# Optimization experiments

Hardware: AMD Instinct MI355X
Metric: run time of the kernel (lower is better)

## Reference

```python
import jax, jax.numpy as jnp
import numpy as np

N_NODES = 51200
N_GRAPHS = 64
NODES_PER_GRAPH = 800
N_EDGES = 819200
DIM_IN = 128
DIM_HIDDEN = 64
HEADS = 3
DIM_OUT = 64


def leaky(x, slope):
    return jnp.where(x >= 0, x, slope * x)


def setup_inputs() -> dict:
    key = jax.random.key(0)
    ks = jax.random.split(key, 12)
    s = lambda fan_in: 1.0 / np.sqrt(fan_in)
    X = jax.random.normal(ks[0], (N_NODES, DIM_IN), dtype=jnp.float32)
    edge_indices = jax.random.randint(ks[1], (2, N_EDGES), 0, N_NODES, dtype=jnp.int32)
    ptr = (jnp.arange(N_GRAPHS + 1, dtype=jnp.int32) * NODES_PER_GRAPH)
    # linearSeq: Linear(dim_in, dim_hidden) + LeakyReLU
    W1 = jax.random.uniform(ks[2], (DIM_IN, DIM_HIDDEN), jnp.float32, -s(DIM_IN), s(DIM_IN))
    b1 = jax.random.uniform(ks[3], (DIM_HIDDEN,), jnp.float32, -s(DIM_IN), s(DIM_IN))
    # GATConv params: lin_src/lin_dst (no bias), att_src/att_dst, bias (concat=False -> out_channels)
    W_src = jax.random.uniform(ks[4], (DIM_HIDDEN, HEADS * DIM_HIDDEN), jnp.float32, -s(DIM_HIDDEN), s(DIM_HIDDEN))
    W_dst = jax.random.uniform(ks[5], (DIM_HIDDEN, HEADS * DIM_HIDDEN), jnp.float32, -s(DIM_HIDDEN), s(DIM_HIDDEN))
    att_src = jax.random.normal(ks[6], (HEADS, DIM_HIDDEN), dtype=jnp.float32) * 0.1
    att_dst = jax.random.normal(ks[7], (HEADS, DIM_HIDDEN), dtype=jnp.float32) * 0.1
    gat_bias = jnp.zeros((DIM_HIDDEN,), dtype=jnp.float32)
    # linear_final: Linear(2*dim_hidden, dim_out)
    Wf = jax.random.uniform(ks[8], (2 * DIM_HIDDEN, DIM_OUT), jnp.float32, -s(2 * DIM_HIDDEN), s(2 * DIM_HIDDEN))
    bf = jax.random.uniform(ks[9], (DIM_OUT,), jnp.float32, -s(2 * DIM_HIDDEN), s(2 * DIM_HIDDEN))
    return {"X": X, "W1": W1, "b1": b1, "W_src": W_src, "W_dst": W_dst,
            "att_src": att_src, "att_dst": att_dst, "gat_bias": gat_bias,
            "Wf": Wf, "bf": bf, "edge_indices": edge_indices, "ptr": ptr}


def reference(X, W1, b1, W_src, W_dst, att_src, att_dst, gat_bias, Wf, bf, edge_indices, ptr):
    N = X.shape[0]
    src, dst = edge_indices[0], edge_indices[1]  # message flows src -> dst
    # input projection
    h = leaky(X @ W1 + b1, 0.01)                                  # [N, DH]
    # GATConv (heads=3, concat=False, add_self_loops=False)
    x_src = (h @ W_src).reshape(N, HEADS, DIM_HIDDEN)             # [N, H, C]
    x_dst = (h @ W_dst).reshape(N, HEADS, DIM_HIDDEN)
    a_src = jnp.einsum('nhc,hc->nh', x_src, att_src)              # [N, H]
    a_dst = jnp.einsum('nhc,hc->nh', x_dst, att_dst)
    logits = leaky(a_src[src] + a_dst[dst], 0.2)                  # [E, H]
    # segment softmax over incoming edges of each target node
    m = jax.ops.segment_max(logits, dst, num_segments=N)          # [N, H]
    e = jnp.exp(logits - m[dst])
    denom = jax.ops.segment_sum(e, dst, num_segments=N)           # [N, H]
    attn = e / denom[dst]                                         # [E, H]
    msg = x_src[src] * attn[..., None]                            # [E, H, C]
    agg = jax.ops.segment_sum(msg, dst, num_segments=N)           # [N, H, C]
    out = agg.mean(axis=1) + gat_bias                             # concat=False -> head mean
    # final head
    cat = jnp.concatenate([h, out], axis=1)                       # [N, 2*DH]
    y = leaky(cat, 0.01) @ Wf + bf                                # [N, DO]
    # aggregate_using_ptr: mean-pool nodes per graph using CSR ptr
    node_graph = jnp.searchsorted(ptr, jnp.arange(N), side='right') - 1
    sums = jax.ops.segment_sum(y, node_graph, num_segments=ptr.shape[0] - 1)
    counts = (ptr[1:] - ptr[:-1]).astype(y.dtype)
    pooled = sums / counts[:, None]                               # [n_graphs, DO]
    return pooled, attn
```

## Files before the change

### kernel.cpp

```cpp
#include <hip/hip_runtime.h>
#include <hip/hip_bf16.h>

#define N_NODES   51200
#define N_GRAPHS  64
#define N_EDGES   819200
#define DIM_IN    128
#define DH        64
#define HEADS     3
#define DIM_OUT   64
#define CAP       96
#define NPART     8
#define PART_SZ   (N_NODES / NPART)
#define PBUF_CAP  131072
#define BIN_BLOCKS  (N_EDGES / 2048)
#define PREP_BLOCKS 116
#define SC2_BLOCKS  (NPART * (PBUF_CAP / 2048))
#define K1_BLOCKS   (N_NODES / 64)

typedef __hip_bfloat16 bf16;
typedef short bf16x8 __attribute__((ext_vector_type(8)));
typedef float f32x4  __attribute__((ext_vector_type(4)));

__device__ __forceinline__ float b2f(bf16 x) { return __bfloat162float(x); }
__device__ __forceinline__ bf16  f2b(float x) { return __float2bfloat16(x); }
__device__ __forceinline__ short f2bs(float x) { return (short)__bfloat16_as_ushort(f2b(x)); }
__device__ __forceinline__ float leaky(float x, float s) { return x >= 0.f ? x : s * x; }
__device__ __forceinline__ float ldin(const void* p, size_t i, int f32) {
    return f32 ? ((const float*)p)[i] : b2f(((const bf16*)p)[i]);
}
__device__ __forceinline__ bf16x8 ld8(const void* p, size_t i, int f32) {
    if (!f32) return *((const bf16x8*)((const short*)p + i));
    const float* f = (const float*)p + i;
    bf16x8 r;
    #pragma unroll
    for (int j = 0; j < 8; ++j) r[j] = f2bs(f[j]);
    return r;
}

__global__ __launch_bounds__(256) void detect_kernel(const unsigned short* __restrict__ Xu,
                                                     int* __restrict__ flag) {
    __shared__ int cnt;
    int tid = threadIdx.x;
    if (tid == 0) cnt = 0;
    __syncthreads();
    int local = 0;
    for (int i = tid * 2; i < 8192; i += 512) {
        unsigned e = (Xu[i] >> 7) & 0xFF;
        if (e >= 110 && e <= 135) local++;
    }
    atomicAdd(&cnt, local);
    __syncthreads();
    if (tid == 0) *flag = (cnt < 2048) ? 1 : 0;
}

__global__ __launch_bounds__(256) void k_bin_prep(const int* __restrict__ src,
                                                  const int* __restrict__ dst,
                                                  int* __restrict__ pcur,
                                                  unsigned* __restrict__ pbuf,
                                                  const void* __restrict__ W1,
                                                  const void* __restrict__ Wsrc,
                                                  const void* __restrict__ Wdst,
                                                  const void* __restrict__ Wf,
                                                  const void* __restrict__ att_src,
                                                  const void* __restrict__ att_dst,
                                                  const int* __restrict__ flagp,
                                                  short* __restrict__ W1t,
                                                  short* __restrict__ Wspt,
                                                  short* __restrict__ Wft,
                                                  short* __restrict__ Wat) {
    if (blockIdx.x < BIN_BLOCKS) {
        __shared__ int cnt[NPART];
        __shared__ int base[NPART];
        const int tid = threadIdx.x;
        if (tid < NPART) cnt[tid] = 0;
        __syncthreads();
        const int e0 = blockIdx.x * 2048;
        unsigned pk[8]; int pp[8]; int rr[8];
        #pragma unroll
        for (int t = 0; t < 8; ++t) {
            int e = e0 + t * 256 + tid;
            int s = src[e], d = dst[e];
            int p = d / PART_SZ;
            pk[t] = ((unsigned)s << 16) | (unsigned)d;
            pp[t] = p;
            rr[t] = atomicAdd(&cnt[p], 1);
        }
        __syncthreads();
        if (tid < NPART) base[tid] = atomicAdd(&pcur[tid], cnt[tid]);
        __syncthreads();
        #pragma unroll
        for (int t = 0; t < 8; ++t) {
            int p = pp[t];
            int o = base[p] + rr[t];
            if (o < PBUF_CAP) pbuf[(size_t)p * PBUF_CAP + o] = pk[t];
        }
        return;
    }
    const int f32 = *flagp;
    int idx = (blockIdx.x - BIN_BLOCKS) * 256 + threadIdx.x;
    if (idx < 8192) {
        int n = idx >> 7, k = idx & 127;
        W1t[idx] = f2bs(ldin(W1, (size_t)k * 64 + n, f32));
    } else if (idx < 20480) {
        int j = idx - 8192;
        int col = j / 192;
        int rem = j - col * 192;
        int hh = rem >> 6, kk = rem & 63;
        Wspt[j] = f2bs(ldin(Wsrc, (size_t)kk * 192 + hh * 64 + col, f32) * (1.0f / 3.0f));
    } else if (idx < 28672) {
        int j = idx - 20480;
        int n = j >> 7, k = j & 127;
        Wft[j] = f2bs(ldin(Wf, (size_t)k * 64 + n, f32));
    } else if (idx < 29696) {
        int j = idx - 28672;
        int n = j >> 6, k = j & 63;
        float v = 0.f;
        if (n < 3) {
            for (int c = 0; c < 64; ++c)
                v += ldin(Wsrc, (size_t)k * 192 + n * 64 + c, f32) * ldin(att_src, n * 64 + c, f32);
        } else if (n < 6) {
            for (int c = 0; c < 64; ++c)
                v += ldin(Wdst, (size_t)k * 192 + (n - 3) * 64 + c, f32) * ldin(att_dst, (n - 3) * 64 + c, f32);
        }
        Wat[j] = f2bs(v);
    }
}

__global__ __launch_bounds__(256) void k_scatter_k1(const unsigned* __restrict__ pbuf,
                                                    const int* __restrict__ pcur,
                                                    int* __restrict__ cursor,
                                                    unsigned short* __restrict__ bucket,
                                                    const void* __restrict__ X,
                                                    const short* __restrict__ W1t,
                                                    const short* __restrict__ Wat,
                                                    const void* __restrict__ b1,
                                                    const int* __restrict__ flagp,
                                                    bf16* __restrict__ h_bf,
                                                    unsigned char* __restrict__ h8,
                                                    float* __restrict__ a_src4,
                                                    float* __restrict__ a_dst4) {
    if (blockIdx.x < SC2_BLOCKS) {
        const int p = blockIdx.x & (NPART - 1);
        const int slice = blockIdx.x >> 3;
        const int pc = min(pcur[p], PBUF_CAP);
        const unsigned* pb = pbuf + (size_t)p * PBUF_CAP;
        const int base = slice * 2048 + threadIdx.x;
        #pragma unroll
        for (int t = 0; t < 8; ++t) {
            int i = base + t * 256;
            if (i < pc) {
                unsigned pk = pb[i];
                int d = (int)(pk & 0xFFFFu);
                int pos = atomicAdd(&cursor[d], 1);
                if (pos < CAP) bucket[(size_t)d * CAP + pos] = (unsigned short)(pk >> 16);
            }
        }
        return;
    }
    const int f32 = *flagp;
    __shared__ short hs[64 * 72];
    const int tid  = threadIdx.x;
    const int w    = tid >> 6;
    const int lane = tid & 63;
    const int lm   = lane & 15;
    const int q    = lane >> 4;
    const int row0 = (blockIdx.x - SC2_BLOCKS) * 64;

    const float bias = ldin(b1, w * 16 + lm, f32);
    for (int mt = 0; mt < 4; ++mt) {
        f32x4 acc = {0.f, 0.f, 0.f, 0.f};
        #pragma unroll
        for (int kc = 0; kc < 4; ++kc) {
            bf16x8 a = ld8(X, (size_t)(row0 + mt * 16 + lm) * 128 + kc * 32 + q * 8, f32);
            bf16x8 b = *((const bf16x8*)(W1t + (size_t)(w * 16 + lm) * 128 + kc * 32 + q * 8));
            acc = __builtin_amdgcn_mfma_f32_16x16x32_bf16(a, b, acc, 0, 0, 0);
        }
        #pragma unroll
        for (int r = 0; r < 4; ++r) {
            int row = mt * 16 + q * 4 + r;
            float v = leaky(acc[r] + bias, 0.01f);
            short hv = f2bs(v);
            hs[row * 72 + w * 16 + lm] = hv;
            h_bf[(size_t)(row0 + row) * 64 + w * 16 + lm] = __ushort_as_bfloat16((unsigned short)hv);
            h8[(size_t)(row0 + row) * 64 + w * 16 + lm] =
                (unsigned char)__builtin_amdgcn_cvt_pk_fp8_f32(v, 0.f, 0, false);
        }
    }
    __syncthreads();

    {
        const int mt = w;
        bf16x8 a0  = *((const bf16x8*)(hs + (mt * 16 + lm) * 72 + q * 8));
        bf16x8 a1  = *((const bf16x8*)(hs + (mt * 16 + lm) * 72 + 32 + q * 8));
        bf16x8 b0  = *((const bf16x8*)(Wat + (size_t)lm * 64 + q * 8));
        bf16x8 b1v = *((const bf16x8*)(Wat + (size_t)lm * 64 + 32 + q * 8));
        f32x4 acca = {0.f, 0.f, 0.f, 0.f};
        acca = __builtin_amdgcn_mfma_f32_16x16x32_bf16(a0, b0, acca, 0, 0, 0);
        acca = __builtin_amdgcn_mfma_f32_16x16x32_bf16(a1, b1v, acca, 0, 0, 0);
        if (lm < 6) {
            #pragma unroll
            for (int r = 0; r < 4; ++r) {
                int row = row0 + mt * 16 + q * 4 + r;
                if (lm < 3) a_src4[(size_t)row * 4 + lm] = acca[r];
                else        a_dst4[(size_t)row * 4 + (lm - 3)] = acca[r];
            }
        }
    }
}

__global__ __launch_bounds__(256) void edge_kernel(const unsigned short* __restrict__ bucket,
                                                   const int* __restrict__ cursor,
                                                   const float* __restrict__ a_src4,
                                                   const float* __restrict__ a_dst4,
                                                   const unsigned char* __restrict__ h8,
                                                   float4* __restrict__ dstinfo,
                                                   bf16* __restrict__ wagg) {
    const int lane = threadIdx.x & 63;
    const int w = threadIdx.x >> 6;
    const int n = blockIdx.x * 4 + w;
    const int dg = min(cursor[n], CAP);
    const float4 ad = ((const float4*)a_dst4)[n];
    __shared__ float4 buf[4][64];
    float den0 = 0.f, den1 = 0.f, den2 = 0.f;
    float acc0 = 0.f, acc1 = 0.f, acc2 = 0.f;
    for (int c0 = 0; c0 < dg; c0 += 64) {
        int cnt = min(64, dg - c0);
        if (lane < cnt) {
            int s = bucket[n * CAP + c0 + lane];
            const float4 as = ((const float4*)a_src4)[s];
            float e0 = __expf(leaky(as.x + ad.x, 0.2f));
            float e1 = __expf(leaky(as.y + ad.y, 0.2f));
            float e2 = __expf(leaky(as.z + ad.z, 0.2f));
            den0 += e0; den1 += e1; den2 += e2;
            buf[w][lane] = make_float4(e0, e1, e2, __int_as_float(s));
        }
        asm volatile("s_waitcnt lgkmcnt(0)" ::: "memory");
        int j = 0;
        for (; j + 8 <= cnt; j += 8) {
            float4 r[8]; int hv[8];
            #pragma unroll
            for (int u = 0; u < 8; ++u) r[u] = buf[w][j + u];
            #pragma unroll
            for (int u = 0; u < 8; ++u)
                hv[u] = (int)h8[(((unsigned)__float_as_int(r[u].w)) << 6) | (unsigned)lane];
            #pragma unroll
            for (int u = 0; u < 8; ++u) {
                float f = __builtin_amdgcn_cvt_f32_fp8(hv[u], 0);
                acc0 += r[u].x * f; acc1 += r[u].y * f; acc2 += r[u].z * f;
            }
        }
        for (; j < cnt; ++j) {
            float4 r = buf[w][j];
            int hvv = (int)h8[(((unsigned)__float_as_int(r.w)) << 6) | (unsigned)lane];
            float f = __builtin_amdgcn_cvt_f32_fp8(hvv, 0);
            acc0 += r.x * f; acc1 += r.y * f; acc2 += r.z * f;
        }
    }
    #pragma unroll
    for (int off = 32; off >= 1; off >>= 1) {
        den0 += __shfl_xor(den0, off);
        den1 += __shfl_xor(den1, off);
        den2 += __shfl_xor(den2, off);
    }
    float inv0 = den0 > 0.f ? 1.f / den0 : 0.f;
    float inv1 = den1 > 0.f ? 1.f / den1 : 0.f;
    float inv2 = den2 > 0.f ? 1.f / den2 : 0.f;
    size_t wb = (size_t)n * 192;
    wagg[wb + lane]       = f2b(acc0 * inv0);
    wagg[wb + 64 + lane]  = f2b(acc1 * inv1);
    wagg[wb + 128 + lane] = f2b(acc2 * inv2);
    if (lane == 0) {
        dstinfo[(size_t)n * 2 + 0] = make_float4(ad.x, ad.y, ad.z, 0.f);
        dstinfo[(size_t)n * 2 + 1] = make_float4(inv0, inv1, inv2, 0.f);
    }
}

__global__ __launch_bounds__(256) void attn_g3_kernel(const int* __restrict__ src,
                                                      const int* __restrict__ dst,
                                                      const float* __restrict__ a_src4,
                                                      const float4* __restrict__ dstinfo,
                                                      const bf16* __restrict__ h_bf,
                                                      const bf16* __restrict__ wagg,
                                                      const short* __restrict__ Wspt,
                                                      const short* __restrict__ Wft,
                                                      const void* __restrict__ gat_bias,
                                                      const void* __restrict__ bfv,
                                                      const int* __restrict__ flagp,
                                                      bf16* __restrict__ y_bf,
                                                      void* __restrict__ d_out) {
    const int f32 = *flagp;
    __shared__ short cs[64 * 136];
    if (blockIdx.x < N_EDGES / 256) {
        int e = blockIdx.x * 256 + threadIdx.x;
        int s = src[e], d = dst[e];
        const float4 as = ((const float4*)a_src4)[s];
        const float4 ad = dstinfo[(size_t)d * 2 + 0];
        const float4 cv = dstinfo[(size_t)d * 2 + 1];
        float a0 = __expf(leaky(as.x + ad.x, 0.2f)) * cv.x;
        float a1 = __expf(leaky(as.y + ad.y, 0.2f)) * cv.y;
        float a2 = __expf(leaky(as.z + ad.z, 0.2f)) * cv.z;
        size_t o = (size_t)N_GRAPHS * DIM_OUT + (size_t)e * 3;
        if (f32) {
            float* p = (float*)d_out;
            p[o] = a0; p[o + 1] = a1; p[o + 2] = a2;
        } else {
            bf16* p = (bf16*)d_out;
            p[o] = f2b(a0); p[o + 1] = f2b(a1); p[o + 2] = f2b(a2);
        }
        return;
    }
    const int bid  = blockIdx.x - N_EDGES / 256;
    const int tid  = threadIdx.x;
    const int w    = tid >> 6;
    const int lane = tid & 63;
    const int lm   = lane & 15;
    const int q    = lane >> 4;
    const int row0 = bid * 64;
    for (int idx = tid; idx < 64 * 64; idx += 256) {
        int r = idx >> 6, k = idx & 63;
        cs[r * 136 + k] = f2bs(leaky(b2f(h_bf[(size_t)(row0 + r) * 64 + k]), 0.01f));
    }
    {
        const int col = w * 16 + lm;
        const float gb = ldin(gat_bias, col, f32);
        for (int mt = 0; mt < 4; ++mt) {
            f32x4 acc = {0.f, 0.f, 0.f, 0.f};
            #pragma unroll
            for (int kc = 0; kc < 6; ++kc) {
                bf16x8 a = *((const bf16x8*)((const short*)wagg + (size_t)(row0 + mt * 16 + lm) * 192 + kc * 32 + q * 8));
                bf16x8 b = *((const bf16x8*)(Wspt + (size_t)col * 192 + kc * 32 + q * 8));
                acc = __builtin_amdgcn_mfma_f32_16x16x32_bf16(a, b, acc, 0, 0, 0);
            }
            #pragma unroll
            for (int r = 0; r < 4; ++r) {
                int row = mt * 16 + q * 4 + r;
                cs[row * 136 + 64 + col] = f2bs(leaky(acc[r] + gb, 0.01f));
            }
        }
    }
    __syncthreads();
    const float bias = ldin(bfv, w * 16 + lm, f32);
    for (int mt = 0; mt < 4; ++mt) {
        f32x4 acc = {0.f, 0.f, 0.f, 0.f};
        #pragma unroll
        for (int kc = 0; kc < 4; ++kc) {
            bf16x8 a = *((const bf16x8*)(cs + (mt * 16 + lm) * 136 + kc * 32 + q * 8));
            bf16x8 b = *((const bf16x8*)(Wft + (size_t)(w * 16 + lm) * 128 + kc * 32 + q * 8));
            acc = __builtin_amdgcn_mfma_f32_16x16x32_bf16(a, b, acc, 0, 0, 0);
        }
        #pragma unroll
        for (int r = 0; r < 4; ++r) {
            int row = row0 + mt * 16 + q * 4 + r;
            y_bf[(size_t)row * 64 + w * 16 + lm] = f2b(acc[r] + bias);
        }
    }
}

__global__ __launch_bounds__(1024) void pool_kernel(const bf16* __restrict__ y_bf,
                                                    const int* __restrict__ ptr,
                                                    const int* __restrict__ flagp,
                                                    void* __restrict__ d_out) {
    __shared__ float part[16][64];
    const int f32 = *flagp;
    const int g = blockIdx.x;
    const int w = threadIdx.x >> 6, lane = threadIdx.x & 63;
    const int lo = ptr[g], hi = ptr[g + 1];
    const int cnt = hi - lo;
    float s = 0.f;
    for (int i = lo + w; i < hi; i += 16) s += b2f(y_bf[(size_t)i * DIM_OUT + lane]);
    part[w][lane] = s;
    __syncthreads();
    if (threadIdx.x < 64) {
        float t = 0.f;
        #pragma unroll
        for (int k = 0; k < 16; ++k) t += part[k][threadIdx.x];
        float v = t / (float)cnt;
        if (f32) ((float*)d_out)[g * DIM_OUT + threadIdx.x] = v;
        else     ((bf16*)d_out)[g * DIM_OUT + threadIdx.x]  = f2b(v);
    }
}

extern "C" void kernel_launch(void* const* d_in, const int* in_sizes, int n_in,
                              void* d_out, int out_size, void* d_ws, size_t ws_size,
                              hipStream_t stream) {
    const void* X        = d_in[0];
    const void* W1       = d_in[1];
    const void* b1       = d_in[2];
    const void* Wsrc     = d_in[3];
    const void* Wdst     = d_in[4];
    const void* att_src  = d_in[5];
    const void* att_dst  = d_in[6];
    const void* gat_bias = d_in[7];
    const void* Wf       = d_in[8];
    const void* bfv      = d_in[9];
    const int*  ei       = (const int*)d_in[10];
    const int*  ptr      = (const int*)d_in[11];
    const int*  src  = ei;
    const int*  dstp = ei + N_EDGES;

    char* ws = (char*)d_ws;
    size_t off_b = 0;
    auto alloc = [&](size_t bytes) -> char* {
        char* p = ws + off_b;
        off_b += (bytes + 255) & ~(size_t)255;
        return p;
    };
    int*     flag    = (int*)    alloc(256);
    short*   W1t     = (short*)  alloc(8192 * 2);
    short*   Wspt    = (short*)  alloc(12288 * 2);
    short*   Wft     = (short*)  alloc(8192 * 2);
    short*   Wat     = (short*)  alloc(1024 * 2);
    bf16*    h_bf    = (bf16*)   alloc((size_t)N_NODES * 64 * 2);
    unsigned char* h8 = (unsigned char*)alloc((size_t)N_NODES * 64);
    float*   a_src4  = (float*)  alloc((size_t)N_NODES * 16);
    float*   a_dst4  = (float*)  alloc((size_t)N_NODES * 16);
    float4*  dstinfo = (float4*) alloc((size_t)N_NODES * 2 * 16);
    bf16*    wagg    = (bf16*)   alloc((size_t)N_NODES * 192 * 2);
    int*     pcur    = (int*)    alloc(256);
    int*     cursor  = (int*)    alloc((size_t)N_NODES * 4);
    unsigned short* bucket = (unsigned short*)alloc((size_t)N_NODES * CAP * 2);
    unsigned* pbuf   = (unsigned*)wagg;
    bf16*    y_bf    = (bf16*)   bucket;
    if (off_b > ws_size) return;

    hipLaunchKernelGGL(detect_kernel, dim3(1), dim3(256), 0, stream,
                       (const unsigned short*)X, flag);
    hipMemsetAsync(pcur, 0, 256 + (size_t)N_NODES * 4, stream);
    hipLaunchKernelGGL(k_bin_prep, dim3(BIN_BLOCKS + PREP_BLOCKS), dim3(256), 0, stream,
                       src, dstp, pcur, pbuf,
                       W1, Wsrc, Wdst, Wf, att_src, att_dst, flag, W1t, Wspt, Wft, Wat);
    hipLaunchKernelGGL(k_scatter_k1, dim3(SC2_BLOCKS + K1_BLOCKS), dim3(256), 0, stream,
                       pbuf, pcur, cursor, bucket,
                       X, W1t, Wat, b1, flag, h_bf, h8, a_src4, a_dst4);
    hipLaunchKernelGGL(edge_kernel, dim3(N_NODES / 4), dim3(256), 0, stream,
                       bucket, cursor, a_src4, a_dst4, h8, dstinfo, wagg);
    hipLaunchKernelGGL(attn_g3_kernel, dim3(N_EDGES / 256 + N_NODES / 64), dim3(256), 0, stream,
                       src, dstp, a_src4, dstinfo, h_bf, wagg, Wspt, Wft,
                       gat_bias, bfv, flag, y_bf, d_out);
    hipLaunchKernelGGL(pool_kernel, dim3(N_GRAPHS), dim3(1024), 0, stream, y_bf, ptr, flag, d_out);
}
```

Baseline: 237.1 us.

## Fuse pooling into final GEMM, merge detect kernel, use LDS counters for scatter

The input-dtype detection moves into the prep blocks of the binning kernel, using a per-block __syncthreads_count plus one extra block that writes the global flag, so the separate detect launch goes away. Edge binning now uses 64 partitions, and each scatter block bins its partition with LDS atomic counters before writing the cursor array, replacing global atomics and the cursor memset. Mean pooling is fused into the final linear stage through per-graph atomic partial sums and a done-counter, so the last block for each graph writes the output. This removes the y_bf round trip and the pool kernel, but adds float atomics, order-dependent summation, and a scatter phase with only 64 blocks.

```diff
diff --git a/kernel.cpp b/kernel.cpp
--- a/kernel.cpp
+++ b/kernel.cpp
@@ -9,12 +9,12 @@
 #define HEADS     3
 #define DIM_OUT   64
 #define CAP       96
-#define NPART     8
+#define NPART     64
 #define PART_SZ   (N_NODES / NPART)
-#define PBUF_CAP  131072
+#define PBUF_CAP  16384
 #define BIN_BLOCKS  (N_EDGES / 2048)
 #define PREP_BLOCKS 116
-#define SC2_BLOCKS  (NPART * (PBUF_CAP / 2048))
+#define SC_BLOCKS   NPART
 #define K1_BLOCKS   (N_NODES / 64)
 
 typedef __hip_bfloat16 bf16;
@@ -37,41 +37,26 @@
     return r;
 }
 
-__global__ __launch_bounds__(256) void detect_kernel(const unsigned short* __restrict__ Xu,
-                                                     int* __restrict__ flag) {
-    __shared__ int cnt;
-    int tid = threadIdx.x;
-    if (tid == 0) cnt = 0;
-    __syncthreads();
-    int local = 0;
-    for (int i = tid * 2; i < 8192; i += 512) {
-        unsigned e = (Xu[i] >> 7) & 0xFF;
-        if (e >= 110 && e <= 135) local++;
-    }
-    atomicAdd(&cnt, local);
-    __syncthreads();
-    if (tid == 0) *flag = (cnt < 2048) ? 1 : 0;
-}
-
 __global__ __launch_bounds__(256) void k_bin_prep(const int* __restrict__ src,
                                                   const int* __restrict__ dst,
                                                   int* __restrict__ pcur,
                                                   unsigned* __restrict__ pbuf,
+                                                  const void* __restrict__ X,
                                                   const void* __restrict__ W1,
                                                   const void* __restrict__ Wsrc,
                                                   const void* __restrict__ Wdst,
                                                   const void* __restrict__ Wf,
                                                   const void* __restrict__ att_src,
                                                   const void* __restrict__ att_dst,
-                                                  const int* __restrict__ flagp,
+                                                  int* __restrict__ flag,
                                                   short* __restrict__ W1t,
                                                   short* __restrict__ Wspt,
                                                   short* __restrict__ Wft,
                                                   short* __restrict__ Wat) {
+    const int tid = threadIdx.x;
     if (blockIdx.x < BIN_BLOCKS) {
         __shared__ int cnt[NPART];
         __shared__ int base[NPART];
-        const int tid = threadIdx.x;
         if (tid < NPART) cnt[tid] = 0;
         __syncthreads();
         const int e0 = blockIdx.x * 2048;
@@ -90,40 +75,56 @@
         __syncthreads();
         #pragma unroll
         for (int t = 0; t < 8; ++t) {
-            int p = pp[t];
-            int o = base[p] + rr[t];
-            if (o < PBUF_CAP) pbuf[(size_t)p * PBUF_CAP + o] = pk[t];
+            int o = base[pp[t]] + rr[t];
+            if (o < PBUF_CAP) pbuf[(size_t)pp[t] * PBUF_CAP + o] = pk[t];
         }
         return;
     }
-    const int f32 = *flagp;
-    int idx = (blockIdx.x - BIN_BLOCKS) * 256 + threadIdx.x;
-    if (idx < 8192) {
-        int n = idx >> 7, k = idx & 127;
-        W1t[idx] = f2bs(ldin(W1, (size_t)k * 64 + n, f32));
-    } else if (idx < 20480) {
-        int j = idx - 8192;
-        int col = j / 192;
-        int rem = j - col * 192;
-        int hh = rem >> 6, kk = rem & 63;
-        Wspt[j] = f2bs(ldin(Wsrc, (size_t)kk * 192 + hh * 64 + col, f32) * (1.0f / 3.0f));
-    } else if (idx < 28672) {
-        int j = idx - 20480;
-        int n = j >> 7, k = j & 127;
-        Wft[j] = f2bs(ldin(Wf, (size_t)k * 64 + n, f32));
-    } else if (idx < 29696) {
-        int j = idx - 28672;
-        int n = j >> 6, k = j & 63;
-        float v = 0.f;
-        if (n < 3) {
-            for (int c = 0; c < 64; ++c)
-                v += ldin(Wsrc, (size_t)k * 192 + n * 64 + c, f32) * ldin(att_src, n * 64 + c, f32);
-        } else if (n < 6) {
-            for (int c = 0; c < 64; ++c)
-                v += ldin(Wdst, (size_t)k * 192 + (n - 3) * 64 + c, f32) * ldin(att_dst, (n - 3) * 64 + c, f32);
-        }
-        Wat[j] = f2bs(v);
-    }
+    if (blockIdx.x < BIN_BLOCKS + PREP_BLOCKS) {
+        unsigned ex = (((const unsigned short*)X)[2 * tid] >> 7) & 0xFF;
+        int c = __syncthreads_count(ex >= 110 && ex <= 135);
+        const int f32 = (c < 128) ? 1 : 0;
+        int idx = (blockIdx.x - BIN_BLOCKS) * 256 + tid;
+        if (idx < 8192) {
+            int n = idx >> 7, k = idx & 127;
+            W1t[idx] = f2bs(ldin(W1, (size_t)k * 64 + n, f32));
+        } else if (idx < 20480) {
+            int j = idx - 8192;
+            int col = j / 192;
+            int rem = j - col * 192;
+            int hh = rem >> 6, kk = rem & 63;
+            Wspt[j] = f2bs(ldin(Wsrc, (size_t)kk * 192 + hh * 64 + col, f32) * (1.0f / 3.0f));
+        } else if (idx < 28672) {
+            int j = idx - 20480;
+            int n = j >> 7, k = j & 127;
+            Wft[j] = f2bs(ldin(Wf, (size_t)k * 64 + n, f32));
+        } else if (idx < 29696) {
+            int j = idx - 28672;
+            int n = j >> 6, k = j & 63;
+            float v = 0.f;
+            if (n < 3) {
+                for (int c2 = 0; c2 < 64; ++c2)
+                    v += ldin(Wsrc, (size_t)k * 192 + n * 64 + c2, f32) * ldin(att_src, n * 64 + c2, f32);
+            } else if (n < 6) {
+                for (int c2 = 0; c2 < 64; ++c2)
+                    v += ldin(Wdst, (size_t)k * 192 + (n - 3) * 64 + c2, f32) * ldin(att_dst, (n - 3) * 64 + c2, f32);
+            }
+            Wat[j] = f2bs(v);
+        }
+        return;
+    }
+    __shared__ int cntp;
+    if (tid == 0) cntp = 0;
+    __syncthreads();
+    int local = 0;
+    const unsigned short* Xu = (const unsigned short*)X;
+    for (int i = tid * 2; i < 8192; i += 512) {
+        unsigned e = (Xu[i] >> 7) & 0xFF;
+        if (e >= 110 && e <= 135) local++;
+    }
+    atomicAdd(&cntp, local);
+    __syncthreads();
+    if (tid == 0) *flag = (cntp < 2048) ? 1 : 0;
 }
 
 __global__ __launch_bounds__(256) void k_scatter_k1(const unsigned* __restrict__ pbuf,
@@ -139,32 +140,32 @@
                                                     unsigned char* __restrict__ h8,
                                                     float* __restrict__ a_src4,
                                                     float* __restrict__ a_dst4) {
-    if (blockIdx.x < SC2_BLOCKS) {
-        const int p = blockIdx.x & (NPART - 1);
-        const int slice = blockIdx.x >> 3;
+    __shared__ short hs[64 * 72];
+    __shared__ int cnt2[PART_SZ];
+    const int tid = threadIdx.x;
+    if (blockIdx.x < SC_BLOCKS) {
+        const int p = blockIdx.x;
+        const int nbase = p * PART_SZ;
+        for (int i = tid; i < PART_SZ; i += 256) cnt2[i] = 0;
+        __syncthreads();
         const int pc = min(pcur[p], PBUF_CAP);
         const unsigned* pb = pbuf + (size_t)p * PBUF_CAP;
-        const int base = slice * 2048 + threadIdx.x;
-        #pragma unroll
-        for (int t = 0; t < 8; ++t) {
-            int i = base + t * 256;
-            if (i < pc) {
-                unsigned pk = pb[i];
-                int d = (int)(pk & 0xFFFFu);
-                int pos = atomicAdd(&cursor[d], 1);
-                if (pos < CAP) bucket[(size_t)d * CAP + pos] = (unsigned short)(pk >> 16);
-            }
-        }
+        for (int i = tid; i < pc; i += 256) {
+            unsigned pk = pb[i];
+            int d = (int)(pk & 0xFFFFu);
+            int pos = atomicAdd(&cnt2[d - nbase], 1);
+            if (pos < CAP) bucket[(size_t)d * CAP + pos] = (unsigned short)(pk >> 16);
+        }
+        __syncthreads();
+        for (int i = tid; i < PART_SZ; i += 256) cursor[nbase + i] = cnt2[i];
         return;
     }
     const int f32 = *flagp;
-    __shared__ short hs[64 * 72];
-    const int tid  = threadIdx.x;
     const int w    = tid >> 6;
     const int lane = tid & 63;
     const int lm   = lane & 15;
     const int q    = lane >> 4;
-    const int row0 = (blockIdx.x - SC2_BLOCKS) * 64;
+    const int row0 = (blockIdx.x - SC_BLOCKS) * 64;
 
     const float bias = ldin(b1, w * 16 + lm, f32);
     for (int mt = 0; mt < 4; ++mt) {
@@ -187,7 +188,6 @@
         }
     }
     __syncthreads();
-
     {
         const int mt = w;
         bf16x8 a0  = *((const bf16x8*)(hs + (mt * 16 + lm) * 72 + q * 8));
@@ -226,7 +226,7 @@
     for (int c0 = 0; c0 < dg; c0 += 64) {
         int cnt = min(64, dg - c0);
         if (lane < cnt) {
-            int s = bucket[n * CAP + c0 + lane];
+            int s = bucket[(size_t)n * CAP + c0 + lane];
             const float4 as = ((const float4*)a_src4)[s];
             float e0 = __expf(leaky(as.x + ad.x, 0.2f));
             float e1 = __expf(leaky(as.y + ad.y, 0.2f));
@@ -286,10 +286,16 @@
                                                       const void* __restrict__ gat_bias,
                                                       const void* __restrict__ bfv,
                                                       const int* __restrict__ flagp,
-                                                      bf16* __restrict__ y_bf,
+                                                      const int* __restrict__ gptr,
+                                                      float* __restrict__ psum,
+                                                      int* __restrict__ done,
                                                       void* __restrict__ d_out) {
     const int f32 = *flagp;
     __shared__ short cs[64 * 136];
+    __shared__ int sptr[N_GRAPHS + 1];
+    __shared__ int rowg_s[64];
+    __shared__ int readyg[64];
+    __shared__ int nready;
     if (blockIdx.x < N_EDGES / 256) {
         int e = blockIdx.x * 256 + threadIdx.x;
         int s = src[e], d = dst[e];
@@ -316,6 +322,15 @@
     const int lm   = lane & 15;
     const int q    = lane >> 4;
     const int row0 = bid * 64;
+    if (tid <= N_GRAPHS) sptr[tid] = gptr[tid];
+    if (tid == 0) nready = 0;
+    __syncthreads();
+    if (tid < 64) {
+        int row = row0 + tid;
+        int lo2 = 0, hi2 = N_GRAPHS;
+        while (hi2 - lo2 > 1) { int mid = (lo2 + hi2) >> 1; if (sptr[mid] <= row) lo2 = mid; else hi2 = mid; }
+        rowg_s[tid] = lo2;
+    }
     for (int idx = tid; idx < 64 * 64; idx += 256) {
         int r = idx >> 6, k = idx & 63;
         cs[r * 136 + k] = f2bs(leaky(b2f(h_bf[(size_t)(row0 + r) * 64 + k]), 0.01f));
@@ -339,44 +354,54 @@
         }
     }
     __syncthreads();
-    const float bias = ldin(bfv, w * 16 + lm, f32);
-    for (int mt = 0; mt < 4; ++mt) {
-        f32x4 acc = {0.f, 0.f, 0.f, 0.f};
-        #pragma unroll
-        for (int kc = 0; kc < 4; ++kc) {
-            bf16x8 a = *((const bf16x8*)(cs + (mt * 16 + lm) * 136 + kc * 32 + q * 8));
-            bf16x8 b = *((const bf16x8*)(Wft + (size_t)(w * 16 + lm) * 128 + kc * 32 + q * 8));
-            acc = __builtin_amdgcn_mfma_f32_16x16x32_bf16(a, b, acc, 0, 0, 0);
-        }
-        #pragma unroll
-        for (int r = 0; r < 4; ++r) {
-            int row = row0 + mt * 16 + q * 4 + r;
-            y_bf[(size_t)row * 64 + w * 16 + lm] = f2b(acc[r] + bias);
-        }
-    }
-}
-
-__global__ __launch_bounds__(1024) void pool_kernel(const bf16* __restrict__ y_bf,
-                                                    const int* __restrict__ ptr,
-                                                    const int* __restrict__ flagp,
-                                                    void* __restrict__ d_out) {
-    __shared__ float part[16][64];
-    const int f32 = *flagp;
-    const int g = blockIdx.x;
-    const int w = threadIdx.x >> 6, lane = threadIdx.x & 63;
-    const int lo = ptr[g], hi = ptr[g + 1];
-    const int cnt = hi - lo;
-    float s = 0.f;
-    for (int i = lo + w; i < hi; i += 16) s += b2f(y_bf[(size_t)i * DIM_OUT + lane]);
-    part[w][lane] = s;
-    __syncthreads();
-    if (threadIdx.x < 64) {
-        float t = 0.f;
-        #pragma unroll
-        for (int k = 0; k < 16; ++k) t += part[k][threadIdx.x];
-        float v = t / (float)cnt;
-        if (f32) ((float*)d_out)[g * DIM_OUT + threadIdx.x] = v;
-        else     ((bf16*)d_out)[g * DIM_OUT + threadIdx.x]  = f2b(v);
+    {
+        const int col = w * 16 + lm;
+        const float bias = ldin(bfv, col, f32);
+        int curg = -1; float runsum = 0.f;
+        for (int mt = 0; mt < 4; ++mt) {
+            f32x4 acc = {0.f, 0.f, 0.f, 0.f};
+            #pragma unroll
+            for (int kc = 0; kc < 4; ++kc) {
+                bf16x8 a = *((const bf16x8*)(cs + (mt * 16 + lm) * 136 + kc * 32 + q * 8));
+                bf16x8 b = *((const bf16x8*)(Wft + (size_t)col * 128 + kc * 32 + q * 8));
+                acc = __builtin_amdgcn_mfma_f32_16x16x32_bf16(a, b, acc, 0, 0, 0);
+            }
+            #pragma unroll
+            for (int r = 0; r < 4; ++r) {
+                int lrow = mt * 16 + q * 4 + r;
+                float v = acc[r] + bias;
+                int g = rowg_s[lrow];
+                if (g != curg) {
+                    if (curg >= 0) atomicAdd(&psum[curg * 64 + col], runsum);
+                    curg = g; runsum = 0.f;
+                }
+                runsum += v;
+            }
+        }
+        if (curg >= 0) atomicAdd(&psum[curg * 64 + col], runsum);
+    }
+    __syncthreads();
+    if (tid == 0) {
+        int g0 = rowg_s[0], g1 = rowg_s[63];
+        int nr = 0;
+        for (int g = g0; g <= g1; ++g) {
+            int lo = sptr[g], hi = sptr[g + 1];
+            if (hi <= lo) continue;
+            int expected = (hi - 1) / 64 - lo / 64 + 1;
+            int old = atomicAdd(&done[g], 1);
+            if (old == expected - 1) readyg[nr++] = g;
+        }
+        nready = nr;
+    }
+    __syncthreads();
+    for (int i = 0; i < nready; ++i) {
+        int g = readyg[i];
+        if (tid < 64) {
+            float s = atomicAdd(&psum[g * 64 + tid], 0.0f);
+            float v = s / (float)(sptr[g + 1] - sptr[g]);
+            if (f32) ((float*)d_out)[g * DIM_OUT + tid] = v;
+            else     ((bf16*)d_out)[g * DIM_OUT + tid]  = f2b(v);
+        }
     }
 }
 
@@ -417,25 +442,23 @@
     float4*  dstinfo = (float4*) alloc((size_t)N_NODES * 2 * 16);
     bf16*    wagg    = (bf16*)   alloc((size_t)N_NODES * 192 * 2);
     int*     pcur    = (int*)    alloc(256);
+    float*   psum    = (float*)  alloc((size_t)N_GRAPHS * 64 * 4);
+    int*     done    = (int*)    alloc(256);
     int*     cursor  = (int*)    alloc((size_t)N_NODES * 4);
     unsigned short* bucket = (unsigned short*)alloc((size_t)N_NODES * CAP * 2);
     unsigned* pbuf   = (unsigned*)wagg;
-    bf16*    y_bf    = (bf16*)   bucket;
     if (off_b > ws_size) return;
 
-    hipLaunchKernelGGL(detect_kernel, dim3(1), dim3(256), 0, stream,
-                       (const unsigned short*)X, flag);
-    hipMemsetAsync(pcur, 0, 256 + (size_t)N_NODES * 4, stream);
-    hipLaunchKernelGGL(k_bin_prep, dim3(BIN_BLOCKS + PREP_BLOCKS), dim3(256), 0, stream,
+    hipMemsetAsync(pcur, 0, 256 + (size_t)N_GRAPHS * 64 * 4 + 256, stream);
+    hipLaunchKernelGGL(k_bin_prep, dim3(BIN_BLOCKS + PREP_BLOCKS + 1), dim3(256), 0, stream,
                        src, dstp, pcur, pbuf,
-                       W1, Wsrc, Wdst, Wf, att_src, att_dst, flag, W1t, Wspt, Wft, Wat);
-    hipLaunchKernelGGL(k_scatter_k1, dim3(SC2_BLOCKS + K1_BLOCKS), dim3(256), 0, stream,
+                       X, W1, Wsrc, Wdst, Wf, att_src, att_dst, flag, W1t, Wspt, Wft, Wat);
+    hipLaunchKernelGGL(k_scatter_k1, dim3(SC_BLOCKS + K1_BLOCKS), dim3(256), 0, stream,
                        pbuf, pcur, cursor, bucket,
                        X, W1t, Wat, b1, flag, h_bf, h8, a_src4, a_dst4);
     hipLaunchKernelGGL(edge_kernel, dim3(N_NODES / 4), dim3(256), 0, stream,
                        bucket, cursor, a_src4, a_dst4, h8, dstinfo, wagg);
     hipLaunchKernelGGL(attn_g3_kernel, dim3(N_EDGES / 256 + N_NODES / 64), dim3(256), 0, stream,
                        src, dstp, a_src4, dstinfo, h_bf, wagg, Wspt, Wft,
-                       gat_bias, bfv, flag, y_bf, d_out);
-    hipLaunchKernelGGL(pool_kernel, dim3(N_GRAPHS), dim3(1024), 0, stream, y_bf, ptr, flag, d_out);
-}
+                       gat_bias, bfv, flag, ptr, psum, done, d_out);
+}
```

After: 217.0 us. 1.09x faster.
